# Optimization experiments

Measured on AMD Instinct MI355X. Metric: run time of the kernel, lower is better.

Reference implementation:

```python
import jax, jax.numpy as jnp
import numpy as np

C = 512
NUM_HEADS = 8


def setup_inputs() -> dict:
    key = jax.random.key(0)
    k1, k2, k3 = jax.random.split(key, 3)
    x = jax.random.normal(k1, (16, C, 32, 32), dtype=jnp.float32)
    # torch Linear(C, 3C) weight shape [3C, C]; y = x @ W.T
    w_qkv = jax.random.normal(k2, (3 * C, C), dtype=jnp.float32) * (1.0 / np.sqrt(C))
    w_out = jax.random.normal(k3, (C, C), dtype=jnp.float32) * (1.0 / np.sqrt(C))
    return {"x": x, "w_qkv": w_qkv, "w_out": w_out}


def reference(x, w_qkv, w_out):
    B, Cc, H, W = x.shape
    S = H * W
    hd = Cc // NUM_HEADS
    # NCHW -> (B, S, C)
    xs = jnp.transpose(x, (0, 2, 3, 1)).reshape(B, S, Cc)
    qkv = jnp.einsum('bsc,dc->bsd', xs, w_qkv).reshape(B, S, 3, NUM_HEADS, hd)
    q = jnp.transpose(qkv[:, :, 0], (0, 2, 1, 3))  # (B, h, S, hd)
    k = jnp.transpose(qkv[:, :, 1], (0, 2, 1, 3))
    v = jnp.transpose(qkv[:, :, 2], (0, 2, 1, 3))
    scale = 1.0 / np.sqrt(hd)
    logits = jnp.einsum('bhqd,bhkd->bhqk', q, k) * scale
    attn = jax.nn.softmax(logits, axis=-1)
    o = jnp.einsum('bhqk,bhkd->bhqd', attn, v)  # (B, h, S, hd)
    o = jnp.transpose(o, (0, 2, 1, 3)).reshape(B, S, Cc)
    out = jnp.einsum('bsc,dc->bsd', o, w_out)
    return jnp.transpose(out.reshape(B, H, W, Cc), (0, 3, 1, 2))
```

## Files before the change

### kernel.cpp

```cpp
#include <hip/hip_runtime.h>
#include <hip/hip_bf16.h>
#include <stdint.h>


typedef __bf16 bf16x8 __attribute__((ext_vector_type(8)));
typedef __bf16 bf16x4 __attribute__((ext_vector_type(4)));
typedef float  f32x4  __attribute__((ext_vector_type(4)));
typedef short  s16x4  __attribute__((ext_vector_type(4)));

#define GLDS16(gptr, lptr)                                                        \
  __builtin_amdgcn_global_load_lds(                                               \
      (const __attribute__((address_space(1))) uint32_t*)(gptr),                  \
      (__attribute__((address_space(3))) uint32_t*)(lptr), 16, 0, 0)

__global__ __launch_bounds__(256) void k_transpose_x(const float* __restrict__ x,
                                                     __bf16* __restrict__ xs) {
  __shared__ float tl[64][36];
  const int s0 = blockIdx.x * 32, c0 = blockIdx.y * 64, b = blockIdx.z;
  const int t = threadIdx.x;
  const int cl = t >> 2, f0 = (t & 3) * 2;
#pragma unroll
  for (int i = 0; i < 2; ++i) {
    const float4 v = *reinterpret_cast<const float4*>(
        x + ((size_t)(b * 512 + c0 + cl)) * 1024 + s0 + (f0 + i) * 4);
    *reinterpret_cast<float4*>(&tl[cl][(f0 + i) * 4]) = v;
  }
  __syncthreads();
  const int sl = t >> 3, ch = t & 7;
  bf16x8 o;
#pragma unroll
  for (int j = 0; j < 8; ++j) o[j] = (__bf16)tl[ch * 8 + j][sl];
  *reinterpret_cast<bf16x8*>(xs + ((size_t)(b * 1024 + s0 + sl)) * 512 + c0 + ch * 8) = o;
}

__global__ __launch_bounds__(256) void k_cast4(const float* __restrict__ in,
                                               __bf16* __restrict__ out) {
  const int i = blockIdx.x * 256 + threadIdx.x;
  const float4 v = reinterpret_cast<const float4*>(in)[i];
  bf16x4 o = {(__bf16)v.x, (__bf16)v.y, (__bf16)v.z, (__bf16)v.w};
  reinterpret_cast<bf16x4*>(out)[i] = o;
}

__device__ __forceinline__ void gemm_core(const __bf16* __restrict__ Ag,
                                          const __bf16* __restrict__ Bg,
                                          int m0, int n0,
                                          __bf16* As, __bf16* Bs,
                                          f32x4 (&acc)[4][4]) {
  const int tid = threadIdx.x, lane = tid & 63, wv = tid >> 6;
  const int wm = (wv >> 1) * 64, wn = (wv & 1) * 64;
  const int lr = lane & 15, lq = lane >> 4;
  const int srow8 = lane >> 3, sc = lane & 7;
  for (int k0 = 0; k0 < 512; k0 += 64) {
    __syncthreads();
#pragma unroll
    for (int t = 0; t < 4; ++t) {
      const int r0 = (wv * 4 + t) * 8;
      const int row = r0 + srow8;
      const int gc = ((sc ^ (row & 7)) * 8);
      GLDS16(Ag + (size_t)(m0 + row) * 512 + k0 + gc, &As[r0 * 64]);
      GLDS16(Bg + (size_t)(n0 + row) * 512 + k0 + gc, &Bs[r0 * 64]);
    }
    __syncthreads();
#pragma unroll
    for (int kk = 0; kk < 64; kk += 32) {
      bf16x8 af[4], bfr[4];
#pragma unroll
      for (int i = 0; i < 4; ++i) {
        const int row = wm + i * 16 + lr;
        af[i] = *reinterpret_cast<const bf16x8*>(
            &As[row * 64 + ((((kk >> 3) + lq) ^ (lr & 7)) * 8)]);
      }
#pragma unroll
      for (int j = 0; j < 4; ++j) {
        const int row = wn + j * 16 + lr;
        bfr[j] = *reinterpret_cast<const bf16x8*>(
            &Bs[row * 64 + ((((kk >> 3) + lq) ^ (lr & 7)) * 8)]);
      }
#pragma unroll
      for (int i = 0; i < 4; ++i)
#pragma unroll
        for (int j = 0; j < 4; ++j)
          acc[i][j] = __builtin_amdgcn_mfma_f32_16x16x32_bf16(af[i], bfr[j], acc[i][j], 0, 0, 0);
    }
  }
}

__global__ __launch_bounds__(256) void k_qkv_gemm(const __bf16* __restrict__ xs,
                                                  const __bf16* __restrict__ wq,
                                                  __bf16* __restrict__ Q,
                                                  __bf16* __restrict__ K,
                                                  __bf16* __restrict__ Vt) {
  __shared__ __align__(16) __bf16 As[128 * 64];
  __shared__ __align__(16) __bf16 Bs[128 * 64];
  const int m0 = blockIdx.x * 128, n0 = blockIdx.y * 128;
  const int tid = threadIdx.x, lane = tid & 63, wv = tid >> 6;
  const int wm = (wv >> 1) * 64, wn = (wv & 1) * 64;
  const int lr = lane & 15, lq = lane >> 4;
  f32x4 acc[4][4] = {};
  gemm_core(xs, wq, m0, n0, As, Bs, acc);
  const float QSC = 0.125f * 1.44269504088896341f;
#pragma unroll
  for (int i = 0; i < 4; ++i) {
    const int mg0 = m0 + wm + i * 16 + lq * 4;
    const int b = mg0 >> 10, s = mg0 & 1023;
#pragma unroll
    for (int j = 0; j < 4; ++j) {
      const int ng = n0 + wn + j * 16 + lr;
      const int t = ng >> 9, h = (ng >> 6) & 7, d = ng & 63;
      if (t == 0) {
#pragma unroll
        for (int r = 0; r < 4; ++r)
          Q[((size_t)((b * 8 + h) * 1024 + s + r)) * 64 + d] = (__bf16)(acc[i][j][r] * QSC);
      } else if (t == 1) {
#pragma unroll
        for (int r = 0; r < 4; ++r)
          K[((size_t)((b * 8 + h) * 1024 + s + r)) * 64 + d] = (__bf16)acc[i][j][r];
      } else {
        bf16x4 pv = {(__bf16)acc[i][j][0], (__bf16)acc[i][j][1],
                     (__bf16)acc[i][j][2], (__bf16)acc[i][j][3]};
        *reinterpret_cast<bf16x4*>(&Vt[((size_t)((b * 8 + h) * 64 + d)) * 1024 + s]) = pv;
      }
    }
  }
}

__global__ __launch_bounds__(128) void k_attn(const __bf16* __restrict__ Q,
                                              const __bf16* __restrict__ K,
                                              const __bf16* __restrict__ Vt,
                                              __bf16* __restrict__ O) {
  __shared__ __align__(16) __bf16 Ks[64 * 64];
  __shared__ __align__(16) __bf16 Vs[64 * 64];
  const int qt = blockIdx.x, h = blockIdx.y, b = blockIdx.z;
  const int tid = threadIdx.x, lane = tid & 63, wv = tid >> 6;
  const int lr = lane & 15, lq = lane >> 4;
  const size_t hbase = (size_t)(b * 8 + h) * 65536;

  bf16x8 qb[2][2];
#pragma unroll
  for (int g = 0; g < 2; ++g)
#pragma unroll
    for (int kx = 0; kx < 2; ++kx)
      qb[g][kx] = *reinterpret_cast<const bf16x8*>(
          Q + hbase + (size_t)(qt * 64 + wv * 32 + g * 16 + lr) * 64 + kx * 32 + lq * 8);

  const int srow8 = lane >> 3, sc = lane & 7;
  int srow[4], sgc[4];
#pragma unroll
  for (int t = 0; t < 4; ++t) {
    srow[t] = wv * 32 + t * 8 + srow8;
    sgc[t] = ((sc ^ (srow[t] & 7)) * 8);
  }
  float l_run[2] = {0.f, 0.f};
  f32x4 o_acc[2][4] = {};

  for (int kt = 0; kt < 16; ++kt) {
    __syncthreads();
#pragma unroll
    for (int t = 0; t < 4; ++t) {
      const int r0 = wv * 32 + t * 8;
      GLDS16(K + hbase + (size_t)(kt * 64 + srow[t]) * 64 + sgc[t], &Ks[r0 * 64]);
      GLDS16(Vt + hbase + (size_t)srow[t] * 1024 + kt * 64 + sgc[t], &Vs[r0 * 64]);
    }
    __syncthreads();
    f32x4 sacc[2][4] = {};
#pragma unroll
    for (int kx = 0; kx < 2; ++kx)
#pragma unroll
      for (int jt = 0; jt < 4; ++jt) {
        const int row = jt * 16 + lr;
        const bf16x8 ka = *reinterpret_cast<const bf16x8*>(
            &Ks[row * 64 + (((kx * 4 + lq) ^ (lr & 7)) * 8)]);
        sacc[0][jt] = __builtin_amdgcn_mfma_f32_16x16x32_bf16(ka, qb[0][kx], sacc[0][jt], 0, 0, 0);
        sacc[1][jt] = __builtin_amdgcn_mfma_f32_16x16x32_bf16(ka, qb[1][kx], sacc[1][jt], 0, 0, 0);
      }
    s16x4 pb[2][4];
#pragma unroll
    for (int g = 0; g < 2; ++g) {
      float ls = 0.f;
#pragma unroll
      for (int c = 0; c < 4; ++c) {
        const float p0 = exp2f(sacc[g][c][0]);
        const float p1 = exp2f(sacc[g][c][1]);
        const float p2 = exp2f(sacc[g][c][2]);
        const float p3 = exp2f(sacc[g][c][3]);
        ls += (p0 + p1) + (p2 + p3);
        bf16x4 pv = {(__bf16)p0, (__bf16)p1, (__bf16)p2, (__bf16)p3};
        pb[g][c] = __builtin_bit_cast(s16x4, pv);
      }
      l_run[g] += ls;
    }
#pragma unroll
    for (int c = 0; c < 4; ++c)
#pragma unroll
      for (int dt = 0; dt < 4; ++dt) {
        const int d = dt * 16 + lr;
        const s16x4 va = *reinterpret_cast<const s16x4*>(
            &Vs[d * 64 + (((2 * c + (lq >> 1)) ^ (lr & 7)) * 8) + (lq & 1) * 4]);
        o_acc[0][dt] = __builtin_amdgcn_mfma_f32_16x16x16bf16_1k(va, pb[0][c], o_acc[0][dt], 0, 0, 0);
        o_acc[1][dt] = __builtin_amdgcn_mfma_f32_16x16x16bf16_1k(va, pb[1][c], o_acc[1][dt], 0, 0, 0);
      }
  }
#pragma unroll
  for (int g = 0; g < 2; ++g) {
    float l1 = l_run[g] + __shfl_xor(l_run[g], 16, 64);
    const float inv = 1.0f / (l1 + __shfl_xor(l1, 32, 64));
    const int sg = qt * 64 + wv * 32 + g * 16 + lr;
#pragma unroll
    for (int dt = 0; dt < 4; ++dt) {
      const int c0 = h * 64 + dt * 16 + lq * 4;
      bf16x4 ov = {(__bf16)(o_acc[g][dt][0] * inv), (__bf16)(o_acc[g][dt][1] * inv),
                   (__bf16)(o_acc[g][dt][2] * inv), (__bf16)(o_acc[g][dt][3] * inv)};
      *reinterpret_cast<bf16x4*>(&O[((size_t)(b * 1024 + sg)) * 512 + c0]) = ov;
    }
  }
}

__global__ __launch_bounds__(256) void k_out_gemm(const __bf16* __restrict__ wo,
                                                  const __bf16* __restrict__ Ob,
                                                  float* __restrict__ out) {
  __shared__ __align__(16) __bf16 As[128 * 64];
  __shared__ __align__(16) __bf16 Bs[128 * 64];
  const int n0 = blockIdx.x * 128, m0 = blockIdx.y * 128;
  const int tid = threadIdx.x, lane = tid & 63, wv = tid >> 6;
  const int wm = (wv >> 1) * 64, wn = (wv & 1) * 64;
  const int lr = lane & 15, lq = lane >> 4;
  f32x4 acc[4][4] = {};
  gemm_core(wo, Ob, m0, n0, As, Bs, acc);
  const int b = n0 >> 10;
#pragma unroll
  for (int i = 0; i < 4; ++i) {
    const int cch = m0 + wm + i * 16 + lq * 4;
#pragma unroll
    for (int j = 0; j < 4; ++j) {
      const int s = (n0 & 1023) + wn + j * 16 + lr;
#pragma unroll
      for (int r = 0; r < 4; ++r)
        out[((size_t)(b * 512 + cch + r)) * 1024 + s] = acc[i][j][r];
    }
  }
}

extern "C" void kernel_launch(void* const* d_in, const int* in_sizes, int n_in,
                              void* d_out, int out_size, void* d_ws, size_t ws_size,
                              hipStream_t stream) {
  const float* x    = (const float*)d_in[0];
  const float* wqkv = (const float*)d_in[1];
  const float* wout = (const float*)d_in[2];
  float* out = (float*)d_out;
  char* ws = (char*)d_ws;
  __bf16* xs    = (__bf16*)(ws);
  __bf16* wqkvb = (__bf16*)(ws + 16777216);
  __bf16* woutb = (__bf16*)(ws + 18350080);
  __bf16* Qb    = (__bf16*)(ws + 18874368);
  __bf16* Kb    = (__bf16*)(ws + 35651584);
  __bf16* Vtb   = (__bf16*)(ws + 52428800);
  __bf16* Ob    = (__bf16*)(ws + 69206016);

  k_transpose_x<<<dim3(32, 8, 16), dim3(256), 0, stream>>>(x, xs);
  k_cast4<<<dim3(768), dim3(256), 0, stream>>>(wqkv, wqkvb);
  k_cast4<<<dim3(256), dim3(256), 0, stream>>>(wout, woutb);
  k_qkv_gemm<<<dim3(128, 12), dim3(256), 0, stream>>>(xs, wqkvb, Qb, Kb, Vtb);
  k_attn<<<dim3(16, 8, 16), dim3(128), 0, stream>>>(Qb, Kb, Vtb, Ob);
  k_out_gemm<<<dim3(128, 4), dim3(256), 0, stream>>>(woutb, Ob, out);
}
```

Before: 224.7 us.

## Split attention keys across wave pairs and read K/V directly from global

The attention kernel now runs 256 threads per block. Two wave groups each process half of the key range and merge their partial output and row-sum through shared memory at the end. The staged LDS copies of K and V, along with their per-tile barriers, are removed; operands are loaded straight from global memory into registers. The exp2 call also switches to the hardware builtin. This removes the per-tile synchronisation and doubles parallelism per block, but it relies on cache hits for K/V reuse and adds an LDS reduction step.

Result: slower. 318.2 us (+41.6%).

```diff
diff --git a/kernel.cpp b/kernel.cpp
--- a/kernel.cpp
+++ b/kernel.cpp
@@ -7,6 +7,12 @@
 typedef __bf16 bf16x4 __attribute__((ext_vector_type(4)));
 typedef float  f32x4  __attribute__((ext_vector_type(4)));
 typedef short  s16x4  __attribute__((ext_vector_type(4)));
+
+#if __has_builtin(__builtin_amdgcn_exp2f)
+#define EXP2(x) __builtin_amdgcn_exp2f(x)
+#else
+#define EXP2(x) exp2f(x)
+#endif
 
 #define GLDS16(gptr, lptr)                                                        \
   __builtin_amdgcn_global_load_lds(                                               \
@@ -124,14 +130,15 @@
   }
 }
 
-__global__ __launch_bounds__(128) void k_attn(const __bf16* __restrict__ Q,
-                                              const __bf16* __restrict__ K,
-                                              const __bf16* __restrict__ Vt,
-                                              __bf16* __restrict__ O) {
-  __shared__ __align__(16) __bf16 Ks[64 * 64];
-  __shared__ __align__(16) __bf16 Vs[64 * 64];
+__global__ __launch_bounds__(256, 3) void k_attn(const __bf16* __restrict__ Q,
+                                                 const __bf16* __restrict__ K,
+                                                 const __bf16* __restrict__ Vt,
+                                                 __bf16* __restrict__ O) {
+  __shared__ f32x4 Lo[16][64];
+  __shared__ float Ll[2][2][64];
   const int qt = blockIdx.x, h = blockIdx.y, b = blockIdx.z;
   const int tid = threadIdx.x, lane = tid & 63, wv = tid >> 6;
+  const int qg = wv & 1, kh = wv >> 1;
   const int lr = lane & 15, lq = lane >> 4;
   const size_t hbase = (size_t)(b * 8 + h) * 65536;
 
@@ -141,35 +148,21 @@
 #pragma unroll
     for (int kx = 0; kx < 2; ++kx)
       qb[g][kx] = *reinterpret_cast<const bf16x8*>(
-          Q + hbase + (size_t)(qt * 64 + wv * 32 + g * 16 + lr) * 64 + kx * 32 + lq * 8);
-
-  const int srow8 = lane >> 3, sc = lane & 7;
-  int srow[4], sgc[4];
-#pragma unroll
-  for (int t = 0; t < 4; ++t) {
-    srow[t] = wv * 32 + t * 8 + srow8;
-    sgc[t] = ((sc ^ (srow[t] & 7)) * 8);
-  }
+          Q + hbase + (size_t)(qt * 64 + qg * 32 + g * 16 + lr) * 64 + kx * 32 + lq * 8);
+
   float l_run[2] = {0.f, 0.f};
   f32x4 o_acc[2][4] = {};
 
-  for (int kt = 0; kt < 16; ++kt) {
-    __syncthreads();
-#pragma unroll
-    for (int t = 0; t < 4; ++t) {
-      const int r0 = wv * 32 + t * 8;
-      GLDS16(K + hbase + (size_t)(kt * 64 + srow[t]) * 64 + sgc[t], &Ks[r0 * 64]);
-      GLDS16(Vt + hbase + (size_t)srow[t] * 1024 + kt * 64 + sgc[t], &Vs[r0 * 64]);
-    }
-    __syncthreads();
+#pragma unroll 2
+  for (int kt = 0; kt < 8; ++kt) {
+    const int kbase = kh * 512 + kt * 64;
     f32x4 sacc[2][4] = {};
 #pragma unroll
     for (int kx = 0; kx < 2; ++kx)
 #pragma unroll
       for (int jt = 0; jt < 4; ++jt) {
-        const int row = jt * 16 + lr;
         const bf16x8 ka = *reinterpret_cast<const bf16x8*>(
-            &Ks[row * 64 + (((kx * 4 + lq) ^ (lr & 7)) * 8)]);
+            K + hbase + (size_t)(kbase + jt * 16 + lr) * 64 + kx * 32 + lq * 8);
         sacc[0][jt] = __builtin_amdgcn_mfma_f32_16x16x32_bf16(ka, qb[0][kx], sacc[0][jt], 0, 0, 0);
         sacc[1][jt] = __builtin_amdgcn_mfma_f32_16x16x32_bf16(ka, qb[1][kx], sacc[1][jt], 0, 0, 0);
       }
@@ -179,10 +172,10 @@
       float ls = 0.f;
 #pragma unroll
       for (int c = 0; c < 4; ++c) {
-        const float p0 = exp2f(sacc[g][c][0]);
-        const float p1 = exp2f(sacc[g][c][1]);
-        const float p2 = exp2f(sacc[g][c][2]);
-        const float p3 = exp2f(sacc[g][c][3]);
+        const float p0 = EXP2(sacc[g][c][0]);
+        const float p1 = EXP2(sacc[g][c][1]);
+        const float p2 = EXP2(sacc[g][c][2]);
+        const float p3 = EXP2(sacc[g][c][3]);
         ls += (p0 + p1) + (p2 + p3);
         bf16x4 pv = {(__bf16)p0, (__bf16)p1, (__bf16)p2, (__bf16)p3};
         pb[g][c] = __builtin_bit_cast(s16x4, pv);
@@ -193,24 +186,37 @@
     for (int c = 0; c < 4; ++c)
 #pragma unroll
       for (int dt = 0; dt < 4; ++dt) {
-        const int d = dt * 16 + lr;
         const s16x4 va = *reinterpret_cast<const s16x4*>(
-            &Vs[d * 64 + (((2 * c + (lq >> 1)) ^ (lr & 7)) * 8) + (lq & 1) * 4]);
+            Vt + hbase + (size_t)(dt * 16 + lr) * 1024 + kbase + c * 16 + lq * 4);
         o_acc[0][dt] = __builtin_amdgcn_mfma_f32_16x16x16bf16_1k(va, pb[0][c], o_acc[0][dt], 0, 0, 0);
         o_acc[1][dt] = __builtin_amdgcn_mfma_f32_16x16x16bf16_1k(va, pb[1][c], o_acc[1][dt], 0, 0, 0);
       }
   }
-#pragma unroll
-  for (int g = 0; g < 2; ++g) {
-    float l1 = l_run[g] + __shfl_xor(l_run[g], 16, 64);
-    const float inv = 1.0f / (l1 + __shfl_xor(l1, 32, 64));
-    const int sg = qt * 64 + wv * 32 + g * 16 + lr;
-#pragma unroll
-    for (int dt = 0; dt < 4; ++dt) {
-      const int c0 = h * 64 + dt * 16 + lq * 4;
-      bf16x4 ov = {(__bf16)(o_acc[g][dt][0] * inv), (__bf16)(o_acc[g][dt][1] * inv),
-                   (__bf16)(o_acc[g][dt][2] * inv), (__bf16)(o_acc[g][dt][3] * inv)};
-      *reinterpret_cast<bf16x4*>(&O[((size_t)(b * 1024 + sg)) * 512 + c0]) = ov;
+  if (kh == 1) {
+#pragma unroll
+    for (int g = 0; g < 2; ++g) {
+      Ll[qg][g][lane] = l_run[g];
+#pragma unroll
+      for (int dt = 0; dt < 4; ++dt) Lo[(qg * 2 + g) * 4 + dt][lane] = o_acc[g][dt];
+    }
+  }
+  __syncthreads();
+  if (kh == 0) {
+#pragma unroll
+    for (int g = 0; g < 2; ++g) {
+      l_run[g] += Ll[qg][g][lane];
+#pragma unroll
+      for (int dt = 0; dt < 4; ++dt) o_acc[g][dt] += Lo[(qg * 2 + g) * 4 + dt][lane];
+      float l1 = l_run[g] + __shfl_xor(l_run[g], 16, 64);
+      const float inv = 1.0f / (l1 + __shfl_xor(l1, 32, 64));
+      const int sg = qt * 64 + qg * 32 + g * 16 + lr;
+#pragma unroll
+      for (int dt = 0; dt < 4; ++dt) {
+        const int c0 = h * 64 + dt * 16 + lq * 4;
+        bf16x4 ov = {(__bf16)(o_acc[g][dt][0] * inv), (__bf16)(o_acc[g][dt][1] * inv),
+                     (__bf16)(o_acc[g][dt][2] * inv), (__bf16)(o_acc[g][dt][3] * inv)};
+        *reinterpret_cast<bf16x4*>(&O[((size_t)(b * 1024 + sg)) * 512 + c0]) = ov;
+      }
     }
   }
 }
@@ -260,6 +266,6 @@
   k_cast4<<<dim3(768), dim3(256), 0, stream>>>(wqkv, wqkvb);
   k_cast4<<<dim3(256), dim3(256), 0, stream>>>(wout, woutb);
   k_qkv_gemm<<<dim3(128, 12), dim3(256), 0, stream>>>(xs, wqkvb, Qb, Kb, Vtb);
-  k_attn<<<dim3(16, 8, 16), dim3(128), 0, stream>>>(Qb, Kb, Vtb, Ob);
+  k_attn<<<dim3(16, 8, 16), dim3(256), 0, stream>>>(Qb, Kb, Vtb, Ob);
   k_out_gemm<<<dim3(128, 4), dim3(256), 0, stream>>>(woutb, Ob, out);
 }
```
